# Kernel tuning notes

Hardware: AMD Instinct MI355X
Metric: run time of the kernel (lower is better)

Reference implementation:

```python
import jax, jax.numpy as jnp
import numpy as np

B, C, H, T_IN, T, EPS = 2048, 512, 256, 64, 32, 1e-5


def _interp_linear(x, t_out):
    # torch F.interpolate mode='linear', align_corners=False on [B,C,T]
    t_in = x.shape[-1]
    scale = t_in / t_out
    src = jnp.maximum((jnp.arange(t_out, dtype=jnp.float32) + 0.5) * scale - 0.5, 0.0)
    i0 = jnp.minimum(jnp.floor(src).astype(jnp.int32), t_in - 1)
    i1 = jnp.minimum(i0 + 1, t_in - 1)
    w1 = (src - i0.astype(jnp.float32))
    return x[:, :, i0] * (1.0 - w1) + x[:, :, i1] * w1


def _dwconv(x, w, pad):
    # depthwise conv1d: x [B,C,T], w [C,1,K]
    return jax.lax.conv_general_dilated(
        x, w, window_strides=(1,), padding=[(pad, pad)],
        dimension_numbers=('NCH', 'OIH', 'NCH'), feature_group_count=x.shape[1])


def _bn(x, g, b, m, v):  # eval-mode BatchNorm1d over channel dim of [B,C,T]
    inv = g / jnp.sqrt(v + EPS)
    return (x - m[:, None]) * inv[:, None] + b[:, None]


def _ln(x, g, b):  # LayerNorm over last dim
    mu = x.mean(-1, keepdims=True)
    var = x.var(-1, keepdims=True)
    return (x - mu) / jnp.sqrt(var + EPS) * g + b


def _gelu(x):
    return jax.nn.gelu(x, approximate=False)


def _attn_weights(feats, lg, lb, w1, b1, w2, b2, temp):
    h = _gelu(_ln(feats, lg, lb) @ w1.T + b1)          # [B,T,H]
    s = (h @ w2.T + b2) / jnp.clip(temp, 0.25, 4.0)    # [B,T,1]
    return jax.nn.softmax(s, axis=1)


def setup_inputs() -> dict:
    key = jax.random.key(0)
    ks = jax.random.split(key, 40)
    n = lambda i, shape, s=0.02: jax.random.normal(ks[i], shape, jnp.float32) * s
    u = lambda i, shape: jax.random.uniform(ks[i], shape, jnp.float32, 0.5, 1.5)
    inp = {
        'x': jax.random.normal(ks[0], (B, C, T_IN), jnp.float32),
        'pos_embed': n(1, (1, T, C)),
        'w3': n(2, (C, 1, 3), 0.1),
        'bn3_g': u(3, (C,)), 'bn3_b': n(4, (C,)), 'bn3_m': n(5, (C,)), 'bn3_v': u(6, (C,)),
        'w5': n(7, (C, 1, 5), 0.1),
        'bn5_g': u(8, (C,)), 'bn5_b': n(9, (C,)), 'bn5_m': n(10, (C,)), 'bn5_v': u(11, (C,)),
        'wmix': n(12, (C, 3 * C), 0.02),
        'bnm_g': u(13, (C,)), 'bnm_b': n(14, (C,)), 'bnm_m': n(15, (C,)), 'bnm_v': u(16, (C,)),
        'ln_g': u(17, (C,)), 'ln_b': n(18, (C,)),
        'ed_ln_g': u(19, (C,)), 'ed_ln_b': n(20, (C,)),
        'ed_w1': n(21, (H, C), 0.04), 'ed_b1': n(22, (H,)),
        'ed_w2': n(23, (1, H), 0.06), 'ed_b2': n(24, (1,)),
        'es_ln_g': u(25, (C,)), 'es_ln_b': n(26, (C,)),
        'es_w1': n(27, (H, C), 0.04), 'es_b1': n(28, (H,)),
        'es_w2': n(29, (1, H), 0.06), 'es_b2': n(30, (1,)),
        'temp_ed': jnp.float32(1.0), 'temp_es': jnp.float32(1.0),
    }
    return inp


def reference(x, pos_embed, w3, bn3_g, bn3_b, bn3_m, bn3_v, w5, bn5_g, bn5_b, bn5_m, bn5_v,
              wmix, bnm_g, bnm_b, bnm_m, bnm_v, ln_g, ln_b,
              ed_ln_g, ed_ln_b, ed_w1, ed_b1, ed_w2, ed_b2,
              es_ln_g, es_ln_b, es_w1, es_b1, es_w2, es_b2, temp_ed, temp_es):
    tf = _interp_linear(x, T)                                 # [B,C,T]
    c3 = _gelu(_bn(_dwconv(tf, w3, 1), bn3_g, bn3_b, bn3_m, bn3_v))
    c5 = _gelu(_bn(_dwconv(tf, w5, 2), bn5_g, bn5_b, bn5_m, bn5_v))
    cat = jnp.concatenate([tf, c3, c5], axis=1)               # [B,3C,T]
    ctx = _gelu(_bn(jnp.einsum('bct,oc->bot', cat, wmix), bnm_g, bnm_b, bnm_m, bnm_v))
    feats = _ln(tf.transpose(0, 2, 1) + ctx.transpose(0, 2, 1) + pos_embed, ln_g, ln_b)  # [B,T,C]
    aw_ed = _attn_weights(feats, ed_ln_g, ed_ln_b, ed_w1, ed_b1, ed_w2, ed_b2, temp_ed)
    aw_es = _attn_weights(feats, es_ln_g, es_ln_b, es_w1, es_b1, es_w2, es_b2, temp_es)
    pair = jnp.concatenate([aw_ed, aw_es], axis=-1)           # [B,T,2]
    w_mean = pair.mean(axis=-1, keepdims=True)                # [B,T,1]
    pooled = (feats * w_mean).sum(axis=1)                     # [B,C]
    return feats, pooled, pair
```

## Files before the change

kernel.cpp:

```cpp
#include <hip/hip_runtime.h>
#include <cstdint>

typedef __bf16 bf16;
typedef __attribute__((ext_vector_type(8))) __bf16 bf16x8;
typedef __attribute__((ext_vector_type(4))) float f32x4;

#define CEPS 1e-5f
#define MROWS 65536
#define NB 2048
#define CDIM 512
#define K3C 1536
#define MKT 24

__device__ __forceinline__ float gelu_f(float x) {
  float x2 = x * x;
  float u = x * (0.7978845608f + 0.0356774081f * x2);
  float e = __expf(2.0f * u);
  float th = 1.0f - __fdividef(2.0f, e + 1.0f);
  return 0.5f * x * (1.0f + th);
}

__device__ __forceinline__ void gload_lds16(const void* g, void* l) {
  using GP = const __attribute__((address_space(1))) void*;
  using LP = __attribute__((address_space(3))) void*;
  __builtin_amdgcn_global_load_lds(reinterpret_cast<GP>(reinterpret_cast<uintptr_t>(g)),
                                   reinterpret_cast<LP>(reinterpret_cast<uintptr_t>(l)),
                                   16, 0, 0);
}

__device__ __forceinline__ int xcd_swz(int bid, int nwg) {
  int q = nwg >> 3, r = nwg & 7;
  int xcd = bid & 7, i = bid >> 3;
  return (xcd < r ? xcd * (q + 1) : r * (q + 1) + (xcd - r) * q) + i;
}

__global__ __launch_bounds__(256) void fold_kernel(
    const float* __restrict__ wmix, const float* __restrict__ bnm_g, const float* __restrict__ bnm_v,
    const float* __restrict__ edg, const float* __restrict__ edb,
    const float* __restrict__ esg, const float* __restrict__ esb,
    const float* __restrict__ w1a, const float* __restrict__ w1b,
    const float* __restrict__ b1a, const float* __restrict__ b1b,
    bf16* __restrict__ wmixf, bf16* __restrict__ w1f, float* __restrict__ b1f) {
  __shared__ float red[4];
  int bid = blockIdx.x, tid = threadIdx.x;
  if (bid < 512) {
    int o = bid;
    float s = bnm_g[o] * rsqrtf(bnm_v[o] + CEPS);
    for (int c = tid; c < K3C; c += 256)
      wmixf[(size_t)o * K3C + c] = (bf16)(wmix[(size_t)o * K3C + c] * s);
  } else {
    int n = bid - 512;
    int half = (n < 256) ? 0 : 1;
    const float* g  = half ? esg : edg;
    const float* lb = half ? esb : edb;
    const float* w1 = half ? w1b : w1a;
    const float* b1 = half ? b1b : b1a;
    int nn = n & 255;
    float dot = 0.f;
    for (int c = tid; c < 512; c += 256) {
      float w = w1[(size_t)nn * 512 + c];
      w1f[(size_t)n * 512 + c] = (bf16)(w * g[c]);
      dot += w * lb[c];
    }
    #pragma unroll
    for (int off = 1; off < 64; off <<= 1) dot += __shfl_xor(dot, off, 64);
    if ((tid & 63) == 0) red[tid >> 6] = dot;
    __syncthreads();
    if (tid == 0) b1f[n] = b1[nn] + red[0] + red[1] + red[2] + red[3];
  }
}

__global__ __launch_bounds__(512) void prep_kernel(
    const float* __restrict__ x,
    const float* __restrict__ w3, const float* __restrict__ bn3g, const float* __restrict__ bn3b,
    const float* __restrict__ bn3m, const float* __restrict__ bn3v,
    const float* __restrict__ w5, const float* __restrict__ bn5g, const float* __restrict__ bn5b,
    const float* __restrict__ bn5m, const float* __restrict__ bn5v,
    bf16* __restrict__ Acat) {
  int b = blockIdx.x, c = threadIdx.x;
  const float4* xp = (const float4*)(x + ((size_t)b * 512 + c) * 64);
  float tf[32];
  #pragma unroll
  for (int i = 0; i < 16; i++) {
    float4 v = xp[i];
    tf[2 * i]     = 0.5f * (v.x + v.y);
    tf[2 * i + 1] = 0.5f * (v.z + v.w);
  }
  float s3 = bn3g[c] * rsqrtf(bn3v[c] + CEPS), t3 = bn3b[c] - bn3m[c] * s3;
  float s5 = bn5g[c] * rsqrtf(bn5v[c] + CEPS), t5 = bn5b[c] - bn5m[c] * s5;
  float w30 = w3[c * 3], w31 = w3[c * 3 + 1], w32 = w3[c * 3 + 2];
  float w50 = w5[c * 5], w51 = w5[c * 5 + 1], w52 = w5[c * 5 + 2], w53 = w5[c * 5 + 3], w54 = w5[c * 5 + 4];
  bf16* Ab = Acat + (size_t)b * 32 * K3C + c;
  #pragma unroll
  for (int t = 0; t < 32; t++) {
    float tm2 = (t >= 2) ? tf[t - 2] : 0.f;
    float tm1 = (t >= 1) ? tf[t - 1] : 0.f;
    float tp1 = (t < 31) ? tf[t + 1] : 0.f;
    float tp2 = (t < 30) ? tf[t + 2] : 0.f;
    float c3 = gelu_f((w30 * tm1 + w31 * tf[t] + w32 * tp1) * s3 + t3);
    float c5 = gelu_f((w50 * tm2 + w51 * tm1 + w52 * tf[t] + w53 * tp1 + w54 * tp2) * s5 + t5);
    Ab[t * K3C]        = (bf16)tf[t];
    Ab[t * K3C + 512]  = (bf16)c3;
    Ab[t * K3C + 1024] = (bf16)c5;
  }
}

#define MFMA1 __builtin_amdgcn_mfma_f32_16x16x32_bf16

#define PHASE(q)                                                              \
  {                                                                           \
    bf16x8 Bf[2][2];                                                          \
    _Pragma("unroll")                                                         \
    for (int i = 0; i < 2; i++) {                                             \
      Bf[i][0] = *(const bf16x8*)(lds + sl + bOff0 + (q) * 16384 + i * 2048); \
      Bf[i][1] = *(const bf16x8*)(lds + sl + bOff1 + (q) * 16384 + i * 2048); \
    }                                                                         \
    __builtin_amdgcn_s_barrier();                                             \
    __builtin_amdgcn_s_setprio(1);                                            \
    _Pragma("unroll")                                                         \
    for (int k2 = 0; k2 < 2; k2++)                                            \
      _Pragma("unroll")                                                       \
      for (int i = 0; i < 2; i++)                                             \
        _Pragma("unroll")                                                     \
        for (int mr = 0; mr < 4; mr++)                                        \
          acc[mr][2 * (q) + i] = MFMA1(Af[mr][k2], Bf[i][k2], acc[mr][2 * (q) + i], 0, 0, 0); \
    __builtin_amdgcn_s_setprio(0);                                            \
    if (stB) stageBq(sl, (q), t + 2);                                         \
  }

__global__ __launch_bounds__(512, 1) void mega_kernel(
    const bf16* __restrict__ Acat, const bf16* __restrict__ Bw, const bf16* __restrict__ w1f,
    const float* __restrict__ bn_g, const float* __restrict__ bn_b,
    const float* __restrict__ bn_m, const float* __restrict__ bn_v,
    const float* __restrict__ pos, const float* __restrict__ lng, const float* __restrict__ lnb,
    const float* __restrict__ b1f, const float* __restrict__ w2a, const float* __restrict__ w2b,
    const float* __restrict__ ta, const float* __restrict__ tb,
    float* __restrict__ feats, float* __restrict__ sE, float* __restrict__ sS) {
  __shared__ char lds[163840];
  int tid = threadIdx.x;
  int wv = tid >> 6, lane = tid & 63;
  int wm = wv >> 2, wn = wv & 3;
  int fr = lane & 15, kq = lane >> 4;
  int mb = xcd_swz(blockIdx.x, gridDim.x);

  const size_t AKB = 3072;
  const char* Ablk = (const char*)Acat + (size_t)mb * 128 * AKB;

  int r8 = tid >> 3;
  int colx = ((tid & 7) << 4) ^ ((r8 & 7) << 4);
  const char* pA = Ablk + (size_t)r8 * AKB + colx;
  int r32 = r8 & 31, st0 = r8 >> 5;
  const char* pB = (const char*)Bw + (size_t)(st0 * 128 + r32) * AKB
                 + (((tid & 7) << 4) ^ ((r32 & 7) << 4));
  const int dstIdx = tid * 16;

  int e0 = (kq << 4) ^ ((fr & 7) << 4);
  int e1 = (64 | (kq << 4)) ^ ((fr & 7) << 4);
  int aB_ = (wm * 64 + fr) * 128;
  int bB_ = 16384 + (wn * 32 + fr) * 128;
  const int aOff0 = aB_ + e0, aOff1 = aB_ + e1;
  const int bOff0 = bB_ + e0, bOff1 = bB_ + e1;

  auto stageA = [&](int slot, int t) {
    char* d = lds + slot + dstIdx;
    const char* s = pA + (size_t)t * 128;
    gload_lds16(s, d);
    gload_lds16(s + 64 * AKB, d + 8192);
  };
  auto stageBq = [&](int slot, int q, int t) {
    char* d = lds + slot + 16384 + q * 16384 + dstIdx;
    const char* s = pB + (size_t)q * 32 * AKB + (size_t)t * 128;
    gload_lds16(s, d);
    gload_lds16(s + 256 * AKB, d + 8192);
  };

  const f32x4 fz = {0.f, 0.f, 0.f, 0.f};
  f32x4 acc[4][8];
  #pragma unroll
  for (int i = 0; i < 4; i++)
    #pragma unroll
    for (int j = 0; j < 8; j++) acc[i][j] = fz;

  stageA(0, 0);
  #pragma unroll
  for (int q = 0; q < 4; q++) stageBq(0, q, 0);
  #pragma unroll
  for (int q = 0; q < 4; q++) stageBq(81920, q, 1);
  asm volatile("s_waitcnt vmcnt(8)" ::: "memory");
  __builtin_amdgcn_s_barrier();

  for (int t = 0; t < MKT; t++) {
    const int sl = (t & 1) * 81920;
    const bool stA = (t + 1 < MKT), stB = (t + 2 < MKT);
    if (stA) stageA(sl ^ 81920, t + 1);
    bf16x8 Af[4][2];
    #pragma unroll
    for (int mr = 0; mr < 4; mr++) {
      Af[mr][0] = *(const bf16x8*)(lds + sl + aOff0 + mr * 2048);
      Af[mr][1] = *(const bf16x8*)(lds + sl + aOff1 + mr * 2048);
    }
    PHASE(0);
    __builtin_amdgcn_s_barrier();
    PHASE(1);
    __builtin_amdgcn_s_barrier();
    PHASE(2);
    __builtin_amdgcn_s_barrier();
    PHASE(3);
    if (t < MKT - 2) {
      asm volatile("s_waitcnt vmcnt(8)" ::: "memory");
    } else if (t == MKT - 2) {
      asm volatile("s_waitcnt vmcnt(0)" ::: "memory");
    }
    __builtin_amdgcn_s_barrier();
  }

  {
    float biasm[8];
    #pragma unroll
    for (int nr = 0; nr < 8; nr++) {
      int n = wn * 128 + nr * 16 + fr;
      float s = bn_g[n] * rsqrtf(bn_v[n] + CEPS);
      biasm[nr] = bn_b[n] - bn_m[n] * s;
    }
    #pragma unroll
    for (int mr = 0; mr < 4; mr++)
      #pragma unroll
      for (int nr = 0; nr < 8; nr++)
        #pragma unroll
        for (int j = 0; j < 4; j++)
          acc[mr][nr][j] = gelu_f(acc[mr][nr][j] + biasm[nr]);
  }
  __syncthreads();
  {
    const char* ptf = Ablk + (size_t)wv * AKB + ((lane * 16) ^ (wv << 4));
    char* d = lds + wv * 1024 + lane * 16;
    #pragma unroll
    for (int l = 0; l < 16; l++) gload_lds16(ptf + (size_t)l * 8 * AKB, d + l * 8192);
  }
  __syncthreads();
  float* sst  = (float*)(lds + 131072);
  float* minv = (float*)(lds + 135168);
  {
    float s1[4][4], s2[4][4];
    #pragma unroll
    for (int mr = 0; mr < 4; mr++)
      #pragma unroll
      for (int j = 0; j < 4; j++) { s1[mr][j] = 0.f; s2[mr][j] = 0.f; }
    #pragma unroll
    for (int mr = 0; mr < 4; mr++)
      #pragma unroll
      for (int j = 0; j < 4; j++) {
        int r = wm * 64 + mr * 16 + kq * 4 + j;
        int swz = (r & 7) << 4;
        #pragma unroll
        for (int nr = 0; nr < 8; nr++) {
          int c = wn * 128 + nr * 16 + fr;
          float tfv = (float)*(const bf16*)(lds + r * 1024 + ((c * 2) ^ swz));
          float z = acc[mr][nr][j] + tfv + pos[(r & 31) * 512 + c];
          acc[mr][nr][j] = z;
          s1[mr][j] += z; s2[mr][j] += z * z;
        }
      }
    #pragma unroll
    for (int mr = 0; mr < 4; mr++)
      #pragma unroll
      for (int j = 0; j < 4; j++)
        #pragma unroll
        for (int off = 1; off < 16; off <<= 1) {
          s1[mr][j] += __shfl_xor(s1[mr][j], off, 64);
          s2[mr][j] += __shfl_xor(s2[mr][j], off, 64);
        }
    if (fr == 0) {
      #pragma unroll
      for (int mr = 0; mr < 4; mr++)
        #pragma unroll
        for (int j = 0; j < 4; j++) {
          int r = wm * 64 + mr * 16 + kq * 4 + j;
          ((float2*)sst)[r * 4 + wn] = make_float2(s1[mr][j], s2[mr][j]);
        }
    }
  }
  __syncthreads();
  if (tid < 128) {
    float a = 0.f, b = 0.f;
    #pragma unroll
    for (int w = 0; w < 4; w++) { float2 v = ((float2*)sst)[tid * 4 + w]; a += v.x; b += v.y; }
    float mu = a * (1.f / 512.f);
    float var = b * (1.f / 512.f) - mu * mu;
    ((float2*)minv)[tid] = make_float2(mu, rsqrtf(var + CEPS));
  }
  __syncthreads();
  {
    float g_[8], b_[8];
    #pragma unroll
    for (int nr = 0; nr < 8; nr++) {
      int c = wn * 128 + nr * 16 + fr;
      g_[nr] = lng[c]; b_[nr] = lnb[c];
    }
    float t1[4][4], t2[4][4];
    #pragma unroll
    for (int mr = 0; mr < 4; mr++)
      #pragma unroll
      for (int j = 0; j < 4; j++) { t1[mr][j] = 0.f; t2[mr][j] = 0.f; }
    #pragma unroll
    for (int mr = 0; mr < 4; mr++)
      #pragma unroll
      for (int j = 0; j < 4; j++) {
        int r = wm * 64 + mr * 16 + kq * 4 + j;
        float2 mi = ((float2*)minv)[r];
        #pragma unroll
        for (int nr = 0; nr < 8; nr++) {
          int c = wn * 128 + nr * 16 + fr;
          float f = (acc[mr][nr][j] - mi.x) * mi.y * g_[nr] + b_[nr];
          acc[mr][nr][j] = f;
          feats[((size_t)mb * 128 + r) * 512 + c] = f;
          t1[mr][j] += f; t2[mr][j] += f * f;
        }
      }
    #pragma unroll
    for (int mr = 0; mr < 4; mr++)
      #pragma unroll
      for (int j = 0; j < 4; j++)
        #pragma unroll
        for (int off = 1; off < 16; off <<= 1) {
          t1[mr][j] += __shfl_xor(t1[mr][j], off, 64);
          t2[mr][j] += __shfl_xor(t2[mr][j], off, 64);
        }
    if (fr == 0) {
      #pragma unroll
      for (int mr = 0; mr < 4; mr++)
        #pragma unroll
        for (int j = 0; j < 4; j++) {
          int r = wm * 64 + mr * 16 + kq * 4 + j;
          ((float2*)sst)[r * 4 + wn] = make_float2(t1[mr][j], t2[mr][j]);
        }
    }
  }
  __syncthreads();
  if (tid < 128) {
    float a = 0.f, b = 0.f;
    #pragma unroll
    for (int w = 0; w < 4; w++) { float2 v = ((float2*)sst)[tid * 4 + w]; a += v.x; b += v.y; }
    float mu = a * (1.f / 512.f);
    float var = b * (1.f / 512.f) - mu * mu;
    ((float2*)minv)[tid] = make_float2(mu, rsqrtf(var + CEPS));
  }
  __syncthreads();
  #pragma unroll
  for (int mr = 0; mr < 4; mr++)
    #pragma unroll
    for (int j = 0; j < 4; j++) {
      int r = wm * 64 + mr * 16 + kq * 4 + j;
      int swz = (r & 7) << 4;
      float2 mi = ((float2*)minv)[r];
      #pragma unroll
      for (int nr = 0; nr < 8; nr++) {
        int c = wn * 128 + nr * 16 + fr;
        *(bf16*)(lds + r * 1024 + ((c * 2) ^ swz)) = (bf16)((acc[mr][nr][j] - mi.x) * mi.y);
      }
    }
  __syncthreads();
  #pragma unroll
  for (int i = 0; i < 4; i++)
    #pragma unroll
    for (int j = 0; j < 8; j++) acc[i][j] = fz;
  float b1l[8], w2l[8];
  #pragma unroll
  for (int h = 0; h < 2; h++) {
    float tv = fminf(fmaxf(h ? tb[0] : ta[0], 0.25f), 4.0f);
    #pragma unroll
    for (int nr = 0; nr < 4; nr++) {
      int np = wn * 64 + nr * 16 + fr;
      b1l[h * 4 + nr] = b1f[h * 256 + np];
      w2l[h * 4 + nr] = (h ? w2b[np] : w2a[np]) / tv;
    }
  }
  {
    const char* pW = (const char*)w1f + (size_t)r8 * 1024 + colx;
    int azB = (wm * 64 + fr) * 1024;
    int abB = 131072 + (wn * 64 + fr) * 128;
    const int azOff0 = azB + e0, azOff1 = azB + e1;
    const int abOff0 = abB + e0, abOff1 = abB + e1;
    #pragma unroll
    for (int h = 0; h < 2; h++) {
      {
        char* d = lds + 131072 + dstIdx;
        #pragma unroll
        for (int l = 0; l < 4; l++)
          gload_lds16(pW + h * 262144 + l * 65536, d + l * 8192);
      }
      __syncthreads();
      for (int kk = 0; kk < 8; kk++) {
        bf16x8 pf[4];
        if (kk < 7) {
          #pragma unroll
          for (int l = 0; l < 4; l++)
            pf[l] = *(const bf16x8*)(pW + h * 262144 + l * 65536 + (kk + 1) * 128);
        }
        bf16x8 Az[4][2], Bz[4][2];
        #pragma unroll
        for (int mr = 0; mr < 4; mr++) {
          Az[mr][0] = *(const bf16x8*)(lds + azOff0 + mr * 16384 + kk * 128);
          Az[mr][1] = *(const bf16x8*)(lds + azOff1 + mr * 16384 + kk * 128);
        }
        #pragma unroll
        for (int nr = 0; nr < 4; nr++) {
          Bz[nr][0] = *(const bf16x8*)(lds + abOff0 + nr * 2048);
          Bz[nr][1] = *(const bf16x8*)(lds + abOff1 + nr * 2048);
        }
        __builtin_amdgcn_s_setprio(1);
        #pragma unroll
        for (int k2 = 0; k2 < 2; k2++)
          #pragma unroll
          for (int mr = 0; mr < 4; mr++)
            #pragma unroll
            for (int nr = 0; nr < 4; nr++)
              acc[mr][h * 4 + nr] = MFMA1(Az[mr][k2], Bz[nr][k2], acc[mr][h * 4 + nr], 0, 0, 0);
        __builtin_amdgcn_s_setprio(0);
        if (kk < 7) {
          __syncthreads();
          char* d = lds + 131072 + dstIdx;
          #pragma unroll
          for (int l = 0; l < 4; l++) *(bf16x8*)(d + l * 8192) = pf[l];
          __syncthreads();
        }
      }
      __syncthreads();
    }
  }
  {
    float pE[4][4], pS[4][4];
    #pragma unroll
    for (int mr = 0; mr < 4; mr++)
      #pragma unroll
      for (int j = 0; j < 4; j++) { pE[mr][j] = 0.f; pS[mr][j] = 0.f; }
    #pragma unroll
    for (int mr = 0; mr < 4; mr++)
      #pragma unroll
      for (int j = 0; j < 4; j++)
        #pragma unroll
        for (int q8 = 0; q8 < 8; q8++) {
          float hh = gelu_f(acc[mr][q8][j] + b1l[q8]) * w2l[q8];
          if (q8 < 4) pE[mr][j] += hh; else pS[mr][j] += hh;
        }
    #pragma unroll
    for (int mr = 0; mr < 4; mr++)
      #pragma unroll
      for (int j = 0; j < 4; j++)
        #pragma unroll
        for (int off = 1; off < 16; off <<= 1) {
          pE[mr][j] += __shfl_xor(pE[mr][j], off, 64);
          pS[mr][j] += __shfl_xor(pS[mr][j], off, 64);
        }
    float* sstE = (float*)(lds + 131072);
    float* sstS = (float*)(lds + 133120);
    if (fr == 0) {
      #pragma unroll
      for (int mr = 0; mr < 4; mr++)
        #pragma unroll
        for (int j = 0; j < 4; j++) {
          int r = wm * 64 + mr * 16 + kq * 4 + j;
          sstE[r * 4 + wn] = pE[mr][j];
          sstS[r * 4 + wn] = pS[mr][j];
        }
    }
    __syncthreads();
    if (tid < 128) {
      float aE = sstE[tid * 4] + sstE[tid * 4 + 1] + sstE[tid * 4 + 2] + sstE[tid * 4 + 3];
      float aS = sstS[tid * 4] + sstS[tid * 4 + 1] + sstS[tid * 4 + 2] + sstS[tid * 4 + 3];
      sE[(size_t)mb * 128 + tid] = aE;
      sS[(size_t)mb * 128 + tid] = aS;
    }
  }
}

__global__ __launch_bounds__(256) void final_kernel(
    const float* __restrict__ sE, const float* __restrict__ sS,
    const float* __restrict__ feats, float* __restrict__ pair, float* __restrict__ pooled) {
  __shared__ float wmL[32];
  int b = blockIdx.x, tid = threadIdx.x;
  if (tid < 32) {
    float vE = sE[(size_t)b * 32 + tid], vS = sS[(size_t)b * 32 + tid];
    float mE = vE, mS = vS;
    #pragma unroll
    for (int off = 1; off < 32; off <<= 1) {
      mE = fmaxf(mE, __shfl_xor(mE, off, 32));
      mS = fmaxf(mS, __shfl_xor(mS, off, 32));
    }
    float eE = expf(vE - mE), eS = expf(vS - mS);
    float sumE = eE, sumS = eS;
    #pragma unroll
    for (int off = 1; off < 32; off <<= 1) {
      sumE += __shfl_xor(sumE, off, 32);
      sumS += __shfl_xor(sumS, off, 32);
    }
    float awE = eE / sumE, awS = eS / sumS;
    size_t pidx = ((size_t)b * 32 + tid) * 2;
    pair[pidx] = awE;
    pair[pidx + 1] = awS;
    wmL[tid] = 0.5f * (awE + awS);
  }
  __syncthreads();
  {
    int c = tid * 2;
    float a0 = 0.f, a1 = 0.f;
    #pragma unroll
    for (int t = 0; t < 32; t++) {
      float2 v = *(const float2*)&feats[((size_t)b * 32 + t) * 512 + c];
      float w = wmL[t];
      a0 += v.x * w; a1 += v.y * w;
    }
    *(float2*)&pooled[(size_t)b * 512 + c] = make_float2(a0, a1);
  }
}

extern "C" void kernel_launch(void* const* d_in, const int* in_sizes, int n_in,
                              void* d_out, int out_size, void* d_ws, size_t ws_size,
                              hipStream_t stream) {
  const float* x     = (const float*)d_in[0];
  const float* pos   = (const float*)d_in[1];
  const float* w3    = (const float*)d_in[2];
  const float* bn3g  = (const float*)d_in[3];
  const float* bn3b  = (const float*)d_in[4];
  const float* bn3m  = (const float*)d_in[5];
  const float* bn3v  = (const float*)d_in[6];
  const float* w5    = (const float*)d_in[7];
  const float* bn5g  = (const float*)d_in[8];
  const float* bn5b  = (const float*)d_in[9];
  const float* bn5m  = (const float*)d_in[10];
  const float* bn5v  = (const float*)d_in[11];
  const float* wmix  = (const float*)d_in[12];
  const float* bnmg  = (const float*)d_in[13];
  const float* bnmb  = (const float*)d_in[14];
  const float* bnmm  = (const float*)d_in[15];
  const float* bnmv  = (const float*)d_in[16];
  const float* lng   = (const float*)d_in[17];
  const float* lnb   = (const float*)d_in[18];
  const float* edlng = (const float*)d_in[19];
  const float* edlnb = (const float*)d_in[20];
  const float* edw1  = (const float*)d_in[21];
  const float* edb1  = (const float*)d_in[22];
  const float* edw2  = (const float*)d_in[23];
  const float* eslng = (const float*)d_in[25];
  const float* eslnb = (const float*)d_in[26];
  const float* esw1  = (const float*)d_in[27];
  const float* esb1  = (const float*)d_in[28];
  const float* esw2  = (const float*)d_in[29];
  const float* ted   = (const float*)d_in[31];
  const float* tes   = (const float*)d_in[32];

  char* ws = (char*)d_ws;
  bf16* Acat  = (bf16*)ws;
  bf16* wmixf = (bf16*)(ws + 201326592);
  bf16* w1f   = (bf16*)(ws + 202899456);
  float* b1f  = (float*)(ws + 203423744);
  float* sEb  = (float*)(ws + 203425792);
  float* sSb  = (float*)(ws + 203687936);

  float* feats  = (float*)d_out;
  float* pooled = feats + 33554432;
  float* pair   = pooled + 1048576;

  fold_kernel<<<1024, 256, 0, stream>>>(wmix, bnmg, bnmv, edlng, edlnb, eslng, eslnb,
                                        edw1, esw1, edb1, esb1, wmixf, w1f, b1f);
  prep_kernel<<<NB, 512, 0, stream>>>(x, w3, bn3g, bn3b, bn3m, bn3v,
                                      w5, bn5g, bn5b, bn5m, bn5v, Acat);
  mega_kernel<<<MROWS / 128, 512, 0, stream>>>(
      Acat, wmixf, w1f, bnmg, bnmb, bnmm, bnmv, pos, lng, lnb,
      b1f, edw2, esw2, ted, tes, feats, sEb, sSb);
  final_kernel<<<NB, 256, 0, stream>>>(sEb, sSb, feats, pair, pooled);
}
```

Measured before the change: 380.0 us.

## Fuse softmax and pooling into mega kernel; stream W1 from registers; stage x via LDS

The final softmax/pooling kernel is folded into the mega kernel's epilogue, so the 128-row block (4 batches) computes the attention weights and the pooled output from the normalized activations already in LDS. This removes the re-read of feats from global memory and one launch. The attention-MLP GEMM now loads W1 fragments straight from global into registers with a one-step prefetch, replacing the LDS staging and its barriers. The prep kernel also stages x through padded LDS to get coalesced loads. The risks are extra register pressure in the mega kernel and the cost of reading uncached W1 from global memory in every block.

```diff
diff --git a/kernel.cpp b/kernel.cpp
--- a/kernel.cpp
+++ b/kernel.cpp
@@ -77,12 +77,21 @@
     const float* __restrict__ w5, const float* __restrict__ bn5g, const float* __restrict__ bn5b,
     const float* __restrict__ bn5m, const float* __restrict__ bn5v,
     bf16* __restrict__ Acat) {
-  int b = blockIdx.x, c = threadIdx.x;
-  const float4* xp = (const float4*)(x + ((size_t)b * 512 + c) * 64);
+  __shared__ float4 xs[8704];
+  int b = blockIdx.x, tid = threadIdx.x;
+  const float4* xg = (const float4*)(x + (size_t)b * 512 * 64);
+  #pragma unroll
+  for (int i = 0; i < 16; i++) {
+    int idx4 = i * 512 + tid;
+    xs[(idx4 >> 4) * 17 + (idx4 & 15)] = xg[idx4];
+  }
+  __syncthreads();
+  int c = tid;
+  const float4* xr = xs + c * 17;
   float tf[32];
   #pragma unroll
   for (int i = 0; i < 16; i++) {
-    float4 v = xp[i];
+    float4 v = xr[i];
     tf[2 * i]     = 0.5f * (v.x + v.y);
     tf[2 * i + 1] = 0.5f * (v.z + v.w);
   }
@@ -135,7 +144,7 @@
     const float* __restrict__ pos, const float* __restrict__ lng, const float* __restrict__ lnb,
     const float* __restrict__ b1f, const float* __restrict__ w2a, const float* __restrict__ w2b,
     const float* __restrict__ ta, const float* __restrict__ tb,
-    float* __restrict__ feats, float* __restrict__ sE, float* __restrict__ sS) {
+    float* __restrict__ feats, float* __restrict__ pair, float* __restrict__ pooled) {
   __shared__ char lds[163840];
   int tid = threadIdx.x;
   int wv = tid >> 6, lane = tid & 63;
@@ -365,129 +374,83 @@
     #pragma unroll
     for (int j = 0; j < 8; j++) acc[i][j] = fz;
   float b1l[8], w2l[8];
-  #pragma unroll
-  for (int h = 0; h < 2; h++) {
-    float tv = fminf(fmaxf(h ? tb[0] : ta[0], 0.25f), 4.0f);
-    #pragma unroll
-    for (int nr = 0; nr < 4; nr++) {
-      int np = wn * 64 + nr * 16 + fr;
-      b1l[h * 4 + nr] = b1f[h * 256 + np];
-      w2l[h * 4 + nr] = (h ? w2b[np] : w2a[np]) / tv;
-    }
-  }
-  {
-    const char* pW = (const char*)w1f + (size_t)r8 * 1024 + colx;
-    int azB = (wm * 64 + fr) * 1024;
-    int abB = 131072 + (wn * 64 + fr) * 128;
-    const int azOff0 = azB + e0, azOff1 = azB + e1;
-    const int abOff0 = abB + e0, abOff1 = abB + e1;
-    #pragma unroll
-    for (int h = 0; h < 2; h++) {
-      {
-        char* d = lds + 131072 + dstIdx;
-        #pragma unroll
-        for (int l = 0; l < 4; l++)
-          gload_lds16(pW + h * 262144 + l * 65536, d + l * 8192);
+  {
+    float tv = fminf(fmaxf((wn < 2) ? ta[0] : tb[0], 0.25f), 4.0f);
+    #pragma unroll
+    for (int nr = 0; nr < 8; nr++) {
+      int n = wn * 128 + nr * 16 + fr;
+      b1l[nr] = b1f[n];
+      w2l[nr] = ((n < 256) ? w2a[n] : w2b[n - 256]) / tv;
+    }
+  }
+  {
+    const char* pWb = (const char*)w1f + (size_t)(wn * 128 + fr) * 1024 + (kq << 4);
+    const int azB = (wm * 64 + fr) * 1024;
+    const int swz = (fr & 7) << 4;
+    bf16x8 Bp[8];
+    #pragma unroll
+    for (int nr = 0; nr < 8; nr++) Bp[nr] = *(const bf16x8*)(pWb + nr * 16384);
+    #pragma unroll
+    for (int kk = 0; kk < 16; kk++) {
+      bf16x8 Bc[8];
+      #pragma unroll
+      for (int nr = 0; nr < 8; nr++) Bc[nr] = Bp[nr];
+      if (kk < 15) {
+        #pragma unroll
+        for (int nr = 0; nr < 8; nr++)
+          Bp[nr] = *(const bf16x8*)(pWb + nr * 16384 + (kk + 1) * 64);
       }
-      __syncthreads();
-      for (int kk = 0; kk < 8; kk++) {
-        bf16x8 pf[4];
-        if (kk < 7) {
-          #pragma unroll
-          for (int l = 0; l < 4; l++)
-            pf[l] = *(const bf16x8*)(pW + h * 262144 + l * 65536 + (kk + 1) * 128);
-        }
-        bf16x8 Az[4][2], Bz[4][2];
-        #pragma unroll
-        for (int mr = 0; mr < 4; mr++) {
-          Az[mr][0] = *(const bf16x8*)(lds + azOff0 + mr * 16384 + kk * 128);
-          Az[mr][1] = *(const bf16x8*)(lds + azOff1 + mr * 16384 + kk * 128);
-        }
-        #pragma unroll
-        for (int nr = 0; nr < 4; nr++) {
-          Bz[nr][0] = *(const bf16x8*)(lds + abOff0 + nr * 2048);
-          Bz[nr][1] = *(const bf16x8*)(lds + abOff1 + nr * 2048);
-        }
-        __builtin_amdgcn_s_setprio(1);
-        #pragma unroll
-        for (int k2 = 0; k2 < 2; k2++)
-          #pragma unroll
-          for (int mr = 0; mr < 4; mr++)
-            #pragma unroll
-            for (int nr = 0; nr < 4; nr++)
-              acc[mr][h * 4 + nr] = MFMA1(Az[mr][k2], Bz[nr][k2], acc[mr][h * 4 + nr], 0, 0, 0);
-        __builtin_amdgcn_s_setprio(0);
-        if (kk < 7) {
-          __syncthreads();
-          char* d = lds + 131072 + dstIdx;
-          #pragma unroll
-          for (int l = 0; l < 4; l++) *(bf16x8*)(d + l * 8192) = pf[l];
-          __syncthreads();
-        }
-      }
-      __syncthreads();
-    }
-  }
-  {
-    float pE[4][4], pS[4][4];
-    #pragma unroll
-    for (int mr = 0; mr < 4; mr++)
-      #pragma unroll
-      for (int j = 0; j < 4; j++) { pE[mr][j] = 0.f; pS[mr][j] = 0.f; }
-    #pragma unroll
-    for (int mr = 0; mr < 4; mr++)
+      bf16x8 Az[4];
+      #pragma unroll
+      for (int mr = 0; mr < 4; mr++)
+        Az[mr] = *(const bf16x8*)(lds + azB + mr * 16384 + (((kk << 6) + (kq << 4)) ^ swz));
+      __builtin_amdgcn_s_setprio(1);
+      #pragma unroll
+      for (int mr = 0; mr < 4; mr++)
+        #pragma unroll
+        for (int nr = 0; nr < 8; nr++)
+          acc[mr][nr] = MFMA1(Az[mr], Bc[nr], acc[mr][nr], 0, 0, 0);
+      __builtin_amdgcn_s_setprio(0);
+    }
+  }
+  float* sred = (float*)(lds + 131072);
+  {
+    #pragma unroll
+    for (int mr = 0; mr < 4; mr++) {
+      float p[4] = {0.f, 0.f, 0.f, 0.f};
+      #pragma unroll
+      for (int nr = 0; nr < 8; nr++)
+        #pragma unroll
+        for (int j = 0; j < 4; j++)
+          p[j] += gelu_f(acc[mr][nr][j] + b1l[nr]) * w2l[nr];
       #pragma unroll
       for (int j = 0; j < 4; j++)
         #pragma unroll
-        for (int q8 = 0; q8 < 8; q8++) {
-          float hh = gelu_f(acc[mr][q8][j] + b1l[q8]) * w2l[q8];
-          if (q8 < 4) pE[mr][j] += hh; else pS[mr][j] += hh;
-        }
-    #pragma unroll
-    for (int mr = 0; mr < 4; mr++)
-      #pragma unroll
-      for (int j = 0; j < 4; j++)
-        #pragma unroll
-        for (int off = 1; off < 16; off <<= 1) {
-          pE[mr][j] += __shfl_xor(pE[mr][j], off, 64);
-          pS[mr][j] += __shfl_xor(pS[mr][j], off, 64);
-        }
-    float* sstE = (float*)(lds + 131072);
-    float* sstS = (float*)(lds + 133120);
-    if (fr == 0) {
-      #pragma unroll
-      for (int mr = 0; mr < 4; mr++)
+        for (int off = 1; off < 16; off <<= 1)
+          p[j] += __shfl_xor(p[j], off, 64);
+      if (fr == 0) {
         #pragma unroll
         for (int j = 0; j < 4; j++) {
           int r = wm * 64 + mr * 16 + kq * 4 + j;
-          sstE[r * 4 + wn] = pE[mr][j];
-          sstS[r * 4 + wn] = pS[mr][j];
-        }
-    }
-    __syncthreads();
-    if (tid < 128) {
-      float aE = sstE[tid * 4] + sstE[tid * 4 + 1] + sstE[tid * 4 + 2] + sstE[tid * 4 + 3];
-      float aS = sstS[tid * 4] + sstS[tid * 4 + 1] + sstS[tid * 4 + 2] + sstS[tid * 4 + 3];
-      sE[(size_t)mb * 128 + tid] = aE;
-      sS[(size_t)mb * 128 + tid] = aS;
-    }
-  }
-}
-
-__global__ __launch_bounds__(256) void final_kernel(
-    const float* __restrict__ sE, const float* __restrict__ sS,
-    const float* __restrict__ feats, float* __restrict__ pair, float* __restrict__ pooled) {
-  __shared__ float wmL[32];
-  int b = blockIdx.x, tid = threadIdx.x;
-  if (tid < 32) {
-    float vE = sE[(size_t)b * 32 + tid], vS = sS[(size_t)b * 32 + tid];
+          sred[r * 4 + wn] = p[j];
+        }
+      }
+    }
+  }
+  __syncthreads();
+  float* wmu = (float*)(lds + 136192);
+  float* mvv = (float*)(lds + 136704);
+  float* vb  = (float*)(lds + 137216);
+  if (tid < 128) {
+    float vE = sred[tid * 4] + sred[tid * 4 + 1];
+    float vS = sred[tid * 4 + 2] + sred[tid * 4 + 3];
     float mE = vE, mS = vS;
     #pragma unroll
     for (int off = 1; off < 32; off <<= 1) {
       mE = fmaxf(mE, __shfl_xor(mE, off, 32));
       mS = fmaxf(mS, __shfl_xor(mS, off, 32));
     }
-    float eE = expf(vE - mE), eS = expf(vS - mS);
+    float eE = __expf(vE - mE), eS = __expf(vS - mS);
     float sumE = eE, sumS = eS;
     #pragma unroll
     for (int off = 1; off < 32; off <<= 1) {
@@ -495,22 +458,33 @@
       sumS += __shfl_xor(sumS, off, 32);
     }
     float awE = eE / sumE, awS = eS / sumS;
-    size_t pidx = ((size_t)b * 32 + tid) * 2;
+    size_t pidx = ((size_t)mb * 128 + tid) * 2;
     pair[pidx] = awE;
     pair[pidx + 1] = awS;
-    wmL[tid] = 0.5f * (awE + awS);
-  }
-  __syncthreads();
-  {
-    int c = tid * 2;
-    float a0 = 0.f, a1 = 0.f;
-    #pragma unroll
-    for (int t = 0; t < 32; t++) {
-      float2 v = *(const float2*)&feats[((size_t)b * 32 + t) * 512 + c];
-      float w = wmL[t];
-      a0 += v.x * w; a1 += v.y * w;
-    }
-    *(float2*)&pooled[(size_t)b * 512 + c] = make_float2(a0, a1);
+    float w = 0.5f * (awE + awS);
+    float2 mi = ((float2*)minv)[tid];
+    wmu[tid] = __fdividef(w, mi.y);
+    mvv[tid] = w * mi.x;
+  }
+  __syncthreads();
+  if (tid < 4) {
+    float s = 0.f;
+    #pragma unroll
+    for (int i = 0; i < 32; i++) s += mvv[tid * 32 + i];
+    vb[tid] = s;
+  }
+  __syncthreads();
+  {
+    int c = tid;
+    float ps[4] = {0.f, 0.f, 0.f, 0.f};
+    #pragma unroll 8
+    for (int r = 0; r < 128; r++) {
+      float zv = (float)*(const bf16*)(lds + r * 1024 + ((c * 2) ^ ((r & 7) << 4)));
+      ps[r >> 5] += zv * wmu[r];
+    }
+    #pragma unroll
+    for (int b = 0; b < 4; b++)
+      pooled[(size_t)(mb * 4 + b) * 512 + c] = ps[b] + vb[b];
   }
 }
 
@@ -554,8 +528,6 @@
   bf16* wmixf = (bf16*)(ws + 201326592);
   bf16* w1f   = (bf16*)(ws + 202899456);
   float* b1f  = (float*)(ws + 203423744);
-  float* sEb  = (float*)(ws + 203425792);
-  float* sSb  = (float*)(ws + 203687936);
 
   float* feats  = (float*)d_out;
   float* pooled = feats + 33554432;
@@ -567,6 +539,5 @@
                                       w5, bn5g, bn5b, bn5m, bn5v, Acat);
   mega_kernel<<<MROWS / 128, 512, 0, stream>>>(
       Acat, wmixf, w1f, bnmg, bnmb, bnmm, bnmv, pos, lng, lnb,
-      b1f, edw2, esw2, ted, tes, feats, sEb, sSb);
-  final_kernel<<<NB, 256, 0, stream>>>(sEb, sSb, feats, pair, pooled);
-}
+      b1f, edw2, esw2, ted, tes, feats, pair, pooled);
+}
```

Result: slower. 399.6 us (+5.2%).

## Fuse softmax and weighted pooling into the main kernel epilogue

Applied to the files above, without the earlier changes.

Removes the separate final kernel. The softmax over the 32 time steps, the pair output and the pooled sum are now computed inside the main kernel's epilogue, using the bf16 normalized rows still held in LDS plus the saved per-row mean and rstd. This avoids re-reading the full feats tensor from global memory and one kernel launch. In exchange it adds epilogue work and extra barriers to the main kernel, and pooled is now built from bf16 values rebuilt from the LN statistics, which may not exactly match the affine-transformed feats.

```diff
diff --git a/kernel.cpp b/kernel.cpp
--- a/kernel.cpp
+++ b/kernel.cpp
@@ -135,7 +135,7 @@
     const float* __restrict__ pos, const float* __restrict__ lng, const float* __restrict__ lnb,
     const float* __restrict__ b1f, const float* __restrict__ w2a, const float* __restrict__ w2b,
     const float* __restrict__ ta, const float* __restrict__ tb,
-    float* __restrict__ feats, float* __restrict__ sE, float* __restrict__ sS) {
+    float* __restrict__ feats, float* __restrict__ pair, float* __restrict__ pooled) {
   __shared__ char lds[163840];
   int tid = threadIdx.x;
   int wv = tid >> 6, lane = tid & 63;
@@ -359,6 +359,9 @@
         *(bf16*)(lds + r * 1024 + ((c * 2) ^ swz)) = (bf16)((acc[mr][nr][j] - mi.x) * mi.y);
       }
     }
+  __syncthreads();
+  float2 miKeep = make_float2(0.f, 1.f);
+  if (tid < 128) miKeep = ((float2*)minv)[tid];
   __syncthreads();
   #pragma unroll
   for (int i = 0; i < 4; i++)
@@ -428,6 +431,8 @@
       __syncthreads();
     }
   }
+  float* sstE = (float*)(lds + 131072);
+  float* sstS = (float*)(lds + 133120);
   {
     float pE[4][4], pS[4][4];
     #pragma unroll
@@ -452,8 +457,6 @@
           pE[mr][j] += __shfl_xor(pE[mr][j], off, 64);
           pS[mr][j] += __shfl_xor(pS[mr][j], off, 64);
         }
-    float* sstE = (float*)(lds + 131072);
-    float* sstS = (float*)(lds + 133120);
     if (fr == 0) {
       #pragma unroll
       for (int mr = 0; mr < 4; mr++)
@@ -464,30 +467,21 @@
           sstS[r * 4 + wn] = pS[mr][j];
         }
     }
-    __syncthreads();
-    if (tid < 128) {
-      float aE = sstE[tid * 4] + sstE[tid * 4 + 1] + sstE[tid * 4 + 2] + sstE[tid * 4 + 3];
-      float aS = sstS[tid * 4] + sstS[tid * 4 + 1] + sstS[tid * 4 + 2] + sstS[tid * 4 + 3];
-      sE[(size_t)mb * 128 + tid] = aE;
-      sS[(size_t)mb * 128 + tid] = aS;
-    }
-  }
-}
-
-__global__ __launch_bounds__(256) void final_kernel(
-    const float* __restrict__ sE, const float* __restrict__ sS,
-    const float* __restrict__ feats, float* __restrict__ pair, float* __restrict__ pooled) {
-  __shared__ float wmL[32];
-  int b = blockIdx.x, tid = threadIdx.x;
-  if (tid < 32) {
-    float vE = sE[(size_t)b * 32 + tid], vS = sS[(size_t)b * 32 + tid];
+  }
+  __syncthreads();
+  float* wmu = (float*)(lds + 136192);
+  float* mvv = (float*)(lds + 136704);
+  float* vb  = (float*)(lds + 137216);
+  if (tid < 128) {
+    float vE = sstE[tid * 4] + sstE[tid * 4 + 1] + sstE[tid * 4 + 2] + sstE[tid * 4 + 3];
+    float vS = sstS[tid * 4] + sstS[tid * 4 + 1] + sstS[tid * 4 + 2] + sstS[tid * 4 + 3];
     float mE = vE, mS = vS;
     #pragma unroll
     for (int off = 1; off < 32; off <<= 1) {
       mE = fmaxf(mE, __shfl_xor(mE, off, 32));
       mS = fmaxf(mS, __shfl_xor(mS, off, 32));
     }
-    float eE = expf(vE - mE), eS = expf(vS - mS);
+    float eE = __expf(vE - mE), eS = __expf(vS - mS);
     float sumE = eE, sumS = eS;
     #pragma unroll
     for (int off = 1; off < 32; off <<= 1) {
@@ -495,22 +489,32 @@
       sumS += __shfl_xor(sumS, off, 32);
     }
     float awE = eE / sumE, awS = eS / sumS;
-    size_t pidx = ((size_t)b * 32 + tid) * 2;
+    size_t pidx = ((size_t)mb * 128 + tid) * 2;
     pair[pidx] = awE;
     pair[pidx + 1] = awS;
-    wmL[tid] = 0.5f * (awE + awS);
-  }
-  __syncthreads();
-  {
-    int c = tid * 2;
-    float a0 = 0.f, a1 = 0.f;
-    #pragma unroll
-    for (int t = 0; t < 32; t++) {
-      float2 v = *(const float2*)&feats[((size_t)b * 32 + t) * 512 + c];
-      float w = wmL[t];
-      a0 += v.x * w; a1 += v.y * w;
-    }
-    *(float2*)&pooled[(size_t)b * 512 + c] = make_float2(a0, a1);
+    float w = 0.5f * (awE + awS);
+    wmu[tid] = __fdividef(w, miKeep.y);
+    mvv[tid] = w * miKeep.x;
+  }
+  __syncthreads();
+  if (tid < 4) {
+    float s = 0.f;
+    #pragma unroll
+    for (int i = 0; i < 32; i++) s += mvv[tid * 32 + i];
+    vb[tid] = s;
+  }
+  __syncthreads();
+  {
+    int c = tid;
+    float ps[4] = {0.f, 0.f, 0.f, 0.f};
+    #pragma unroll 8
+    for (int r = 0; r < 128; r++) {
+      float zv = (float)*(const bf16*)(lds + r * 1024 + ((c * 2) ^ ((r & 7) << 4)));
+      ps[r >> 5] += zv * wmu[r];
+    }
+    #pragma unroll
+    for (int b = 0; b < 4; b++)
+      pooled[(size_t)(mb * 4 + b) * 512 + c] = ps[b] + vb[b];
   }
 }
 
@@ -554,8 +558,6 @@
   bf16* wmixf = (bf16*)(ws + 201326592);
   bf16* w1f   = (bf16*)(ws + 202899456);
   float* b1f  = (float*)(ws + 203423744);
-  float* sEb  = (float*)(ws + 203425792);
-  float* sSb  = (float*)(ws + 203687936);
 
   float* feats  = (float*)d_out;
   float* pooled = feats + 33554432;
@@ -567,6 +569,5 @@
                                       w5, bn5g, bn5b, bn5m, bn5v, Acat);
   mega_kernel<<<MROWS / 128, 512, 0, stream>>>(
       Acat, wmixf, w1f, bnmg, bnmb, bnmm, bnmv, pos, lng, lnb,
-      b1f, edw2, esw2, ted, tes, feats, sEb, sSb);
-  final_kernel<<<NB, 256, 0, stream>>>(sEb, sSb, feats, pair, pooled);
-}
+      b1f, edw2, esw2, ted, tes, feats, pair, pooled);
+}
```

After: 371.5 us. -2.3%, faster.
